# Kernel tuning notes

Measured on AMD Instinct MI355X. Metric: run time of the kernel, lower is better.

Reference implementation:

```python
import jax, jax.numpy as jnp
import numpy as np


def swish(x):
    return x * jax.nn.sigmoid(x)


def setup_inputs() -> dict:
    key = jax.random.key(0)
    ks = jax.random.split(key, 12)
    b, n, c, h, dg, hid = 4, 512, 256, 8, 6, 16

    def lin(k, i, o):
        return jax.random.normal(k, (i, o), jnp.float32) / np.float32(np.sqrt(i))

    return {
        "pairwise_g": jax.random.normal(ks[0], (b, n, n, dg), jnp.float32),
        "coset_functions": jax.random.normal(ks[1], (b, n, c), jnp.float32),
        "fc_q_w": lin(ks[2], c, c), "fc_q_b": jnp.zeros((c,), jnp.float32),
        "fc_k_w": lin(ks[3], c, c), "fc_k_b": jnp.zeros((c,), jnp.float32),
        "in_w": lin(ks[4], c, c), "in_b": jnp.zeros((c,), jnp.float32),
        "out_w": lin(ks[5], c, c), "out_b": jnp.zeros((c,), jnp.float32),
        "loc_w1": jax.random.normal(ks[6], (h, dg, hid), jnp.float32) / np.float32(np.sqrt(dg)),
        "loc_b1": jnp.zeros((h, hid), jnp.float32),
        "loc_w2": jax.random.normal(ks[7], (h, hid, hid), jnp.float32) / np.float32(np.sqrt(hid)),
        "loc_b2": jnp.zeros((h, hid), jnp.float32),
        "loc_w3": jax.random.normal(ks[8], (h, hid, 1), jnp.float32) / np.float32(np.sqrt(hid)),
        "loc_b3": jnp.zeros((h, 1), jnp.float32),
        "mask": jax.random.randint(ks[9], (4, 512), 0, 2) > 0,
    }


def reference(pairwise_g, coset_functions, fc_q_w, fc_q_b, fc_k_w, fc_k_b,
              in_w, in_b, out_w, out_b,
              loc_w1, loc_b1, loc_w2, loc_b2, loc_w3, loc_b3, mask):
    # nbhd_idx = arange(n) in the original (dense neighborhoods), so all
    # advanced-index gathers are identities and are expressed as broadcasts.
    b, n, c = coset_functions.shape
    h = loc_w1.shape[0]
    d = c // h

    # DotProductKernel: scores scaled by sqrt(embed_dim) = sqrt(c)
    Q = (coset_functions @ fc_q_w + fc_q_b).reshape(b, n, h, d)
    K = (coset_functions @ fc_k_w + fc_k_b).reshape(b, n, h, d)
    A_feat = jnp.einsum('bnhd,bmhd->bnmh', Q, K) / np.float32(np.sqrt(c))  # (b,n,m,h)

    # MultiheadWeightNet location kernel: per-head 3-layer MLP with swish
    # after every linear (LieConv-style LinearBNact blocks), out_dim=1.
    x = swish(jnp.einsum('bnmg,hgk->bnmhk', pairwise_g, loc_w1) + loc_b1)
    x = swish(jnp.einsum('bnmhk,hkj->bnmhj', x, loc_w2) + loc_b2)
    A_loc = swish(jnp.einsum('bnmhk,hko->bnmho', x, loc_w3) + loc_b3)[..., 0]  # (b,n,m,h)

    pre = A_loc + A_feat
    nbhd_mask = mask[:, None, :, None]          # mask over keys j: (b,1,m,1)
    pre = jnp.where(nbhd_mask, pre, jnp.float32(-1e38))
    att = jax.nn.softmax(pre, axis=2)           # softmax over neighbor dim m

    V = (coset_functions @ in_w + in_b).reshape(b, n, h, d)  # input_linear
    out = jnp.einsum('bnmh,bmhd->bnhd', att, V).reshape(b, n, c)
    return out @ out_w + out_b                  # output_linear; (b,n,c_out)
```

## Files before the change

### kernel.cpp

```cpp
#include <hip/hip_runtime.h>
#include <math.h>

namespace {

constexpr int kB = 4, kN = 512, kC = 256, kH = 8, kDG = 6, kHID = 16;

typedef _Float16 half2v __attribute__((ext_vector_type(2)));

__device__ __forceinline__ float swishf(float x) {
    return x * __builtin_amdgcn_rcpf(1.0f + __expf(-x));
}

__device__ __forceinline__ unsigned pk16(float a, float b) {
    unsigned short ha = __builtin_bit_cast(unsigned short, (_Float16)a);
    unsigned short hb = __builtin_bit_cast(unsigned short, (_Float16)b);
    return (unsigned)ha | ((unsigned)hb << 16);
}

__device__ __forceinline__ unsigned pkrtz(float a, float b) {
#if __has_builtin(__builtin_amdgcn_cvt_pkrtz)
    return __builtin_bit_cast(unsigned, __builtin_amdgcn_cvt_pkrtz(a, b));
#else
    return pk16(a, b);
#endif
}

__device__ __forceinline__ float fdot2u(unsigned a, unsigned b, float c) {
#if __has_builtin(__builtin_amdgcn_fdot2)
    return __builtin_amdgcn_fdot2(__builtin_bit_cast(half2v, a),
                                  __builtin_bit_cast(half2v, b), c, false);
#else
    half2v ha = __builtin_bit_cast(half2v, a);
    half2v hb = __builtin_bit_cast(half2v, b);
    return c + (float)ha[0] * (float)hb[0] + (float)ha[1] * (float)hb[1];
#endif
}

__global__ __launch_bounds__(256) void k_qkvc(
    const float* __restrict__ x,
    const float* __restrict__ wq, const float* __restrict__ bq,
    const float* __restrict__ wk, const float* __restrict__ bk,
    const float* __restrict__ wv, const float* __restrict__ bv,
    unsigned* __restrict__ Qh, unsigned* __restrict__ Kh,
    float* __restrict__ V,
    const unsigned char* __restrict__ mraw,
    int* __restrict__ list, int* __restrict__ meta) {
    const int t = threadIdx.x;

    if (blockIdx.x == 512) {
        __shared__ int s_isbool;
        if (t == 0) s_isbool = 0;
        __syncthreads();
        int found = 0;
        for (int i = t; i < kB * kN; i += 256)
            if ((i & 3) && mraw[i]) found = 1;
        if (found) atomicOr(&s_isbool, 1);
        __syncthreads();
        const int isb = s_isbool;
        const int b = t >> 6, lane = t & 63;
        const int* mi = (const int*)mraw;
        int base = 0;
        for (int c = 0; c < 8; ++c) {
            const int m = c * 64 + lane;
            const int idx = b * kN + m;
            const int valid = isb ? (mraw[idx] != 0) : (mi[idx] != 0);
            unsigned long long bal = __ballot(valid);
            int rank = (int)__popcll(bal & ((1ull << lane) - 1ull));
            if (valid) list[b * kN + base + rank] = m;
            base += (int)__popcll(bal);
        }
        for (int i = base + lane; i < kN; i += 64)
            list[b * kN + i] = (base == 0) ? i : 0;
        if (lane == 0) {
            meta[b] = (base == 0) ? kN : base;
            meta[4 + b] = (base == 0);
        }
        return;
    }

    __shared__ float sx[4][kC];
    const int r0 = blockIdx.x * 4;
    #pragma unroll
    for (int r = 0; r < 4; ++r) sx[r][t] = x[(r0 + r) * kC + t];
    __syncthreads();
    float aq[4] = {}, ak[4] = {}, av[4] = {};
    for (int k = 0; k < kC; ++k) {
        const float q = wq[k * kC + t];
        const float kk = wk[k * kC + t];
        const float v = wv[k * kC + t];
        #pragma unroll
        for (int r = 0; r < 4; ++r) {
            aq[r] += sx[r][k] * q;
            ak[r] += sx[r][k] * kk;
            av[r] += sx[r][k] * v;
        }
    }
    const float qb = bq[t], kb = bk[t], vb = bv[t];
    #pragma unroll
    for (int r = 0; r < 4; ++r) {
        const float qv = aq[r] + qb;
        const float kv = ak[r] + kb;
        V[(r0 + r) * kC + t] = av[r] + vb;
        const float qn = __shfl_down(qv, 1);
        const float kn = __shfl_down(kv, 1);
        if ((t & 1) == 0) {
            Qh[(r0 + r) * (kC / 2) + (t >> 1)] = pk16(qv, qn);
            Kh[(r0 + r) * (kC / 2) + (t >> 1)] = pk16(kv, kn);
        }
    }
}

__global__ __launch_bounds__(256, 6) void k_attn(
    const float* __restrict__ G,
    const unsigned* __restrict__ Qh,
    const unsigned* __restrict__ Kh,
    const float* __restrict__ V,
    const float* __restrict__ w1, const float* __restrict__ b1,
    const float* __restrict__ w2, const float* __restrict__ b2,
    const float* __restrict__ w3, const float* __restrict__ b3,
    const int* __restrict__ list, const int* __restrict__ meta,
    float* __restrict__ out) {
    __shared__ __align__(16) unsigned sQh[kC / 2];
    __shared__ __align__(16) unsigned sG[kN][4];
    __shared__ int sList[kN];
    __shared__ __align__(16) unsigned sW1[kH][kHID][4];
    __shared__ __align__(16) unsigned sW2[kH][kHID][8];
    __shared__ float sB1[kH][kHID];
    __shared__ float sB2[kH][kHID];
    __shared__ float sW3[kH][kHID];
    __shared__ float sB3[kH];
    __shared__ float sAtt[kH][kN];
    __shared__ float sInv[kH];

    const int bn = blockIdx.x;
    const int b = bn >> 9;
    const int t = threadIdx.x;

    if (t < kC / 2) sQh[t] = Qh[bn * (kC / 2) + t];
    sList[t] = list[b * kN + t];
    sList[t + 256] = list[b * kN + t + 256];
    #pragma unroll 1
    for (int rep = 0; rep < 2; ++rep) {
        const int m = t + rep * 256;
        const float* gp = G + ((size_t)bn * kN + m) * kDG;
        uint4 gw;
        gw.x = pkrtz(gp[0], gp[1]);
        gw.y = pkrtz(gp[2], gp[3]);
        gw.z = pkrtz(gp[4], gp[5]);
        gw.w = 0;
        *(uint4*)&sG[m][0] = gw;
    }
    if (t < 128) {
        const int h = t >> 4, k = t & 15;
        const float* wp = w1 + (h * kDG) * kHID + k;
        sW1[h][k][0] = pk16(wp[0], wp[16]);
        sW1[h][k][1] = pk16(wp[32], wp[48]);
        sW1[h][k][2] = pk16(wp[64], wp[80]);
        sW1[h][k][3] = 0;
        sB1[h][k] = b1[h * kHID + k];
        sB2[h][k] = b2[h * kHID + k];
        sW3[h][k] = w3[h * kHID + k];
    } else {
        const int t2 = t - 128;
        const int h = t2 >> 4, j = t2 & 15;
        const float* wp = w2 + h * kHID * kHID + j;
        #pragma unroll
        for (int kp = 0; kp < 8; ++kp)
            sW2[h][j][kp] = pk16(wp[(2 * kp) * kHID], wp[(2 * kp + 1) * kHID]);
        if (j == 0) sB3[h] = b3[h];
    }
    const int nv = meta[b];
    const int allm = meta[4 + b];
    __syncthreads();

    #pragma unroll 1
    for (int rep = 0; rep < 2; ++rep) {
        const int mc = t + rep * 256;
        if (mc < nv) {
            const int m = sList[mc];
            const uint4 gw = *(const uint4*)&sG[m][0];
            const unsigned* khrow = Kh + ((size_t)b * kN + m) * (kC / 2);
            #pragma unroll 1
            for (int h = 0; h < kH; ++h) {
                float af = 0.f;
                const uint4* kh4 = (const uint4*)(khrow + h * 16);
                const uint4* qh4 = (const uint4*)&sQh[h * 16];
                #pragma unroll
                for (int i = 0; i < 4; ++i) {
                    const uint4 kv = kh4[i];
                    const uint4 qv = qh4[i];
                    af = fdot2u(kv.x, qv.x, af);
                    af = fdot2u(kv.y, qv.y, af);
                    af = fdot2u(kv.z, qv.z, af);
                    af = fdot2u(kv.w, qv.w, af);
                }
                unsigned xp[8];
                #pragma unroll
                for (int k2 = 0; k2 < 8; ++k2) {
                    const uint4 wa = *(const uint4*)&sW1[h][2 * k2][0];
                    const uint4 wb = *(const uint4*)&sW1[h][2 * k2 + 1][0];
                    float aa = sB1[h][2 * k2], ab = sB1[h][2 * k2 + 1];
                    aa = fdot2u(gw.x, wa.x, aa);
                    aa = fdot2u(gw.y, wa.y, aa);
                    aa = fdot2u(gw.z, wa.z, aa);
                    ab = fdot2u(gw.x, wb.x, ab);
                    ab = fdot2u(gw.y, wb.y, ab);
                    ab = fdot2u(gw.z, wb.z, ab);
                    xp[k2] = pkrtz(swishf(aa), swishf(ab));
                }
                float a3 = sB3[h];
                #pragma unroll
                for (int j = 0; j < kHID; ++j) {
                    const uint4 w0 = ((const uint4*)&sW2[h][j][0])[0];
                    const uint4 w1q = ((const uint4*)&sW2[h][j][0])[1];
                    float acc = sB2[h][j];
                    acc = fdot2u(xp[0], w0.x, acc);
                    acc = fdot2u(xp[1], w0.y, acc);
                    acc = fdot2u(xp[2], w0.z, acc);
                    acc = fdot2u(xp[3], w0.w, acc);
                    acc = fdot2u(xp[4], w1q.x, acc);
                    acc = fdot2u(xp[5], w1q.y, acc);
                    acc = fdot2u(xp[6], w1q.z, acc);
                    acc = fdot2u(xp[7], w1q.w, acc);
                    a3 += swishf(acc) * sW3[h][j];
                }
                sAtt[h][mc] = allm ? 0.f : (swishf(a3) + af * 0.0625f);
            }
        }
    }
    __syncthreads();

    {
        const int hg = t >> 5;
        const int lane = t & 31;
        const int nv4 = (nv + 3) & ~3;
        float mx = -3.4e38f;
        for (int idx = lane; idx < nv; idx += 32)
            mx = fmaxf(mx, sAtt[hg][idx]);
        #pragma unroll
        for (int off = 16; off; off >>= 1)
            mx = fmaxf(mx, __shfl_xor(mx, off));
        float ls = 0.f;
        for (int idx = lane; idx < nv4; idx += 32) {
            const float e = (idx < nv) ? __expf(sAtt[hg][idx] - mx) : 0.f;
            sAtt[hg][idx] = e;
            ls += e;
        }
        #pragma unroll
        for (int off = 16; off; off >>= 1)
            ls += __shfl_xor(ls, off);
        if (lane == 0) sInv[hg] = 1.0f / ls;
    }
    __syncthreads();

    {
        const int h = t >> 5;
        const int dd = t & 31;
        const int nv4 = (nv + 3) & ~3;
        const float* vb = V + (size_t)b * kN * kC + h * 32 + dd;
        float a0 = 0.f, a1 = 0.f, a2 = 0.f, a3 = 0.f;
        for (int mc = 0; mc < nv4; mc += 4) {
            a0 += sAtt[h][mc + 0] * vb[(size_t)sList[mc + 0] * kC];
            a1 += sAtt[h][mc + 1] * vb[(size_t)sList[mc + 1] * kC];
            a2 += sAtt[h][mc + 2] * vb[(size_t)sList[mc + 2] * kC];
            a3 += sAtt[h][mc + 3] * vb[(size_t)sList[mc + 3] * kC];
        }
        out[bn * kC + t] = ((a0 + a1) + (a2 + a3)) * sInv[h];
    }
}

__global__ __launch_bounds__(256) void k_proj(
    const float* __restrict__ x,
    const float* __restrict__ w, const float* __restrict__ bias,
    float* __restrict__ y) {
    __shared__ float sx[8][kC];
    const int r0 = blockIdx.x * 8;
    const int t = threadIdx.x;
    #pragma unroll
    for (int r = 0; r < 8; ++r) sx[r][t] = x[(r0 + r) * kC + t];
    __syncthreads();
    float acc[8] = {};
    for (int k = 0; k < kC; ++k) {
        const float wv = w[k * kC + t];
        #pragma unroll
        for (int r = 0; r < 8; ++r) acc[r] += sx[r][k] * wv;
    }
    const float bb = bias[t];
    #pragma unroll
    for (int r = 0; r < 8; ++r) y[(r0 + r) * kC + t] = acc[r] + bb;
}

}

extern "C" void kernel_launch(void* const* d_in, const int* in_sizes, int n_in,
                              void* d_out, int out_size, void* d_ws, size_t ws_size,
                              hipStream_t stream) {
    (void)in_sizes; (void)n_in; (void)out_size; (void)ws_size;
    const float* G  = (const float*)d_in[0];
    const float* cf = (const float*)d_in[1];
    const float* wq = (const float*)d_in[2];
    const float* bq = (const float*)d_in[3];
    const float* wk = (const float*)d_in[4];
    const float* bk = (const float*)d_in[5];
    const float* wv = (const float*)d_in[6];
    const float* bv = (const float*)d_in[7];
    const float* wo = (const float*)d_in[8];
    const float* bo = (const float*)d_in[9];
    const float* w1 = (const float*)d_in[10];
    const float* b1 = (const float*)d_in[11];
    const float* w2 = (const float*)d_in[12];
    const float* b2 = (const float*)d_in[13];
    const float* w3 = (const float*)d_in[14];
    const float* b3 = (const float*)d_in[15];
    const unsigned char* mraw = (const unsigned char*)d_in[16];

    const int rows = kB * kN;
    unsigned* Qh = (unsigned*)d_ws;
    unsigned* Kh = Qh + (size_t)rows * (kC / 2);
    float* V = (float*)(Kh + (size_t)rows * (kC / 2));
    float* O = V + (size_t)rows * kC;
    int* list = (int*)(O + (size_t)rows * kC);
    int* meta = list + rows;

    k_qkvc<<<513, 256, 0, stream>>>(cf, wq, bq, wk, bk, wv, bv,
                                    Qh, Kh, V, mraw, list, meta);
    k_attn<<<rows, 256, 0, stream>>>(G, Qh, Kh, V, w1, b1, w2, b2, w3, b3,
                                     list, meta, O);
    k_proj<<<rows / 8, 256, 0, stream>>>(O, wo, bo, (float*)d_out);
}
```

Before: 264.3 us.

## Flatten key-head work items across threads and pad shared arrays against bank conflicts

The attention score loop now gives each thread one (key, head) pair from a flattened list of nv*8 items, where before each thread looped over all 8 heads for a key. This balances work when nv is not a multiple of 256 and lets the K loads and weight reads proceed without the serial head loop. Shared arrays (Q, W1, W2, biases, attention scores) get padded row strides so that threads in a wavefront touching different heads avoid LDS bank conflicts. The occupancy hint is lowered from 6 to 4 blocks, which lets the compiler use more registers but may reduce latency hiding. Adjacent lanes now read weights from different heads, so LDS broadcast of a shared address is lost.

```diff
diff --git a/kernel.cpp b/kernel.cpp
--- a/kernel.cpp
+++ b/kernel.cpp
@@ -4,6 +4,12 @@
 namespace {
 
 constexpr int kB = 4, kN = 512, kC = 256, kH = 8, kDG = 6, kHID = 16;
+
+constexpr int S_QH = 20;
+constexpr int S_W1 = 68;
+constexpr int S_W2 = 132;
+constexpr int S_B  = 17;
+constexpr int S_AT = 516;
 
 typedef _Float16 half2v __attribute__((ext_vector_type(2)));
 
@@ -110,7 +116,7 @@
     }
 }
 
-__global__ __launch_bounds__(256, 6) void k_attn(
+__global__ __launch_bounds__(256, 4) void k_attn(
     const float* __restrict__ G,
     const unsigned* __restrict__ Qh,
     const unsigned* __restrict__ Kh,
@@ -120,23 +126,26 @@
     const float* __restrict__ w3, const float* __restrict__ b3,
     const int* __restrict__ list, const int* __restrict__ meta,
     float* __restrict__ out) {
-    __shared__ __align__(16) unsigned sQh[kC / 2];
-    __shared__ __align__(16) unsigned sG[kN][4];
+    __shared__ __align__(16) unsigned sQh[kH * S_QH];
+    __shared__ __align__(16) uint4 sG4[kN];
     __shared__ int sList[kN];
-    __shared__ __align__(16) unsigned sW1[kH][kHID][4];
-    __shared__ __align__(16) unsigned sW2[kH][kHID][8];
-    __shared__ float sB1[kH][kHID];
-    __shared__ float sB2[kH][kHID];
-    __shared__ float sW3[kH][kHID];
+    __shared__ __align__(16) unsigned sW1[kH * S_W1];
+    __shared__ __align__(16) unsigned sW2[kH * S_W2];
+    __shared__ float sB1[kH * S_B];
+    __shared__ float sB2[kH * S_B];
+    __shared__ float sW3[kH * S_B];
     __shared__ float sB3[kH];
-    __shared__ float sAtt[kH][kN];
+    __shared__ float sAtt[kH * S_AT];
     __shared__ float sInv[kH];
 
     const int bn = blockIdx.x;
     const int b = bn >> 9;
     const int t = threadIdx.x;
 
-    if (t < kC / 2) sQh[t] = Qh[bn * (kC / 2) + t];
+    if (t < kH * S_QH) {
+        const int h = t / S_QH, r = t % S_QH;
+        sQh[t] = (r < 16) ? Qh[bn * (kC / 2) + h * 16 + r] : 0u;
+    }
     sList[t] = list[b * kN + t];
     sList[t + 256] = list[b * kN + t + 256];
     #pragma unroll 1
@@ -148,84 +157,82 @@
         gw.y = pkrtz(gp[2], gp[3]);
         gw.z = pkrtz(gp[4], gp[5]);
         gw.w = 0;
-        *(uint4*)&sG[m][0] = gw;
+        sG4[m] = gw;
     }
     if (t < 128) {
         const int h = t >> 4, k = t & 15;
         const float* wp = w1 + (h * kDG) * kHID + k;
-        sW1[h][k][0] = pk16(wp[0], wp[16]);
-        sW1[h][k][1] = pk16(wp[32], wp[48]);
-        sW1[h][k][2] = pk16(wp[64], wp[80]);
-        sW1[h][k][3] = 0;
-        sB1[h][k] = b1[h * kHID + k];
-        sB2[h][k] = b2[h * kHID + k];
-        sW3[h][k] = w3[h * kHID + k];
+        sW1[h * S_W1 + k * 4 + 0] = pk16(wp[0], wp[16]);
+        sW1[h * S_W1 + k * 4 + 1] = pk16(wp[32], wp[48]);
+        sW1[h * S_W1 + k * 4 + 2] = pk16(wp[64], wp[80]);
+        sW1[h * S_W1 + k * 4 + 3] = 0;
+        sB1[h * S_B + k] = b1[h * kHID + k];
+        sB2[h * S_B + k] = b2[h * kHID + k];
+        sW3[h * S_B + k] = w3[h * kHID + k];
     } else {
         const int t2 = t - 128;
         const int h = t2 >> 4, j = t2 & 15;
         const float* wp = w2 + h * kHID * kHID + j;
         #pragma unroll
         for (int kp = 0; kp < 8; ++kp)
-            sW2[h][j][kp] = pk16(wp[(2 * kp) * kHID], wp[(2 * kp + 1) * kHID]);
+            sW2[h * S_W2 + j * 8 + kp] = pk16(wp[(2 * kp) * kHID], wp[(2 * kp + 1) * kHID]);
         if (j == 0) sB3[h] = b3[h];
     }
     const int nv = meta[b];
     const int allm = meta[4 + b];
     __syncthreads();
 
+    const int items = nv * kH;
     #pragma unroll 1
-    for (int rep = 0; rep < 2; ++rep) {
-        const int mc = t + rep * 256;
-        if (mc < nv) {
+    for (int base = 0; base < items; base += 256) {
+        const int idx = base + t;
+        if (idx < items) {
+            const int h = idx & 7;
+            const int mc = idx >> 3;
             const int m = sList[mc];
-            const uint4 gw = *(const uint4*)&sG[m][0];
-            const unsigned* khrow = Kh + ((size_t)b * kN + m) * (kC / 2);
-            #pragma unroll 1
-            for (int h = 0; h < kH; ++h) {
-                float af = 0.f;
-                const uint4* kh4 = (const uint4*)(khrow + h * 16);
-                const uint4* qh4 = (const uint4*)&sQh[h * 16];
-                #pragma unroll
-                for (int i = 0; i < 4; ++i) {
-                    const uint4 kv = kh4[i];
-                    const uint4 qv = qh4[i];
-                    af = fdot2u(kv.x, qv.x, af);
-                    af = fdot2u(kv.y, qv.y, af);
-                    af = fdot2u(kv.z, qv.z, af);
-                    af = fdot2u(kv.w, qv.w, af);
-                }
-                unsigned xp[8];
-                #pragma unroll
-                for (int k2 = 0; k2 < 8; ++k2) {
-                    const uint4 wa = *(const uint4*)&sW1[h][2 * k2][0];
-                    const uint4 wb = *(const uint4*)&sW1[h][2 * k2 + 1][0];
-                    float aa = sB1[h][2 * k2], ab = sB1[h][2 * k2 + 1];
-                    aa = fdot2u(gw.x, wa.x, aa);
-                    aa = fdot2u(gw.y, wa.y, aa);
-                    aa = fdot2u(gw.z, wa.z, aa);
-                    ab = fdot2u(gw.x, wb.x, ab);
-                    ab = fdot2u(gw.y, wb.y, ab);
-                    ab = fdot2u(gw.z, wb.z, ab);
-                    xp[k2] = pkrtz(swishf(aa), swishf(ab));
-                }
-                float a3 = sB3[h];
-                #pragma unroll
-                for (int j = 0; j < kHID; ++j) {
-                    const uint4 w0 = ((const uint4*)&sW2[h][j][0])[0];
-                    const uint4 w1q = ((const uint4*)&sW2[h][j][0])[1];
-                    float acc = sB2[h][j];
-                    acc = fdot2u(xp[0], w0.x, acc);
-                    acc = fdot2u(xp[1], w0.y, acc);
-                    acc = fdot2u(xp[2], w0.z, acc);
-                    acc = fdot2u(xp[3], w0.w, acc);
-                    acc = fdot2u(xp[4], w1q.x, acc);
-                    acc = fdot2u(xp[5], w1q.y, acc);
-                    acc = fdot2u(xp[6], w1q.z, acc);
-                    acc = fdot2u(xp[7], w1q.w, acc);
-                    a3 += swishf(acc) * sW3[h][j];
-                }
-                sAtt[h][mc] = allm ? 0.f : (swishf(a3) + af * 0.0625f);
+            const uint4 gw = sG4[m];
+            const unsigned* khrow = Kh + ((size_t)(b * kN) + m) * (kC / 2) + h * 16;
+            float af = 0.f;
+            #pragma unroll
+            for (int i = 0; i < 4; ++i) {
+                const uint4 kv = ((const uint4*)khrow)[i];
+                const uint4 qv = *(const uint4*)&sQh[h * S_QH + 4 * i];
+                af = fdot2u(kv.x, qv.x, af);
+                af = fdot2u(kv.y, qv.y, af);
+                af = fdot2u(kv.z, qv.z, af);
+                af = fdot2u(kv.w, qv.w, af);
             }
+            unsigned xp[8];
+            #pragma unroll
+            for (int k2 = 0; k2 < 8; ++k2) {
+                const uint4 wa = *(const uint4*)&sW1[h * S_W1 + (2 * k2) * 4];
+                const uint4 wb = *(const uint4*)&sW1[h * S_W1 + (2 * k2 + 1) * 4];
+                float aa = sB1[h * S_B + 2 * k2], ab = sB1[h * S_B + 2 * k2 + 1];
+                aa = fdot2u(gw.x, wa.x, aa);
+                aa = fdot2u(gw.y, wa.y, aa);
+                aa = fdot2u(gw.z, wa.z, aa);
+                ab = fdot2u(gw.x, wb.x, ab);
+                ab = fdot2u(gw.y, wb.y, ab);
+                ab = fdot2u(gw.z, wb.z, ab);
+                xp[k2] = pkrtz(swishf(aa), swishf(ab));
+            }
+            float a3 = sB3[h];
+            #pragma unroll
+            for (int j = 0; j < kHID; ++j) {
+                const uint4 w0 = *(const uint4*)&sW2[h * S_W2 + j * 8];
+                const uint4 w1q = *(const uint4*)&sW2[h * S_W2 + j * 8 + 4];
+                float acc = sB2[h * S_B + j];
+                acc = fdot2u(xp[0], w0.x, acc);
+                acc = fdot2u(xp[1], w0.y, acc);
+                acc = fdot2u(xp[2], w0.z, acc);
+                acc = fdot2u(xp[3], w0.w, acc);
+                acc = fdot2u(xp[4], w1q.x, acc);
+                acc = fdot2u(xp[5], w1q.y, acc);
+                acc = fdot2u(xp[6], w1q.z, acc);
+                acc = fdot2u(xp[7], w1q.w, acc);
+                a3 += swishf(acc) * sW3[h * S_B + j];
+            }
+            sAtt[h * S_AT + mc] = allm ? 0.f : (swishf(a3) + af * 0.0625f);
         }
     }
     __syncthreads();
@@ -236,14 +243,14 @@
         const int nv4 = (nv + 3) & ~3;
         float mx = -3.4e38f;
         for (int idx = lane; idx < nv; idx += 32)
-            mx = fmaxf(mx, sAtt[hg][idx]);
+            mx = fmaxf(mx, sAtt[hg * S_AT + idx]);
         #pragma unroll
         for (int off = 16; off; off >>= 1)
             mx = fmaxf(mx, __shfl_xor(mx, off));
         float ls = 0.f;
         for (int idx = lane; idx < nv4; idx += 32) {
-            const float e = (idx < nv) ? __expf(sAtt[hg][idx] - mx) : 0.f;
-            sAtt[hg][idx] = e;
+            const float e = (idx < nv) ? __expf(sAtt[hg * S_AT + idx] - mx) : 0.f;
+            sAtt[hg * S_AT + idx] = e;
             ls += e;
         }
         #pragma unroll
@@ -260,10 +267,10 @@
         const float* vb = V + (size_t)b * kN * kC + h * 32 + dd;
         float a0 = 0.f, a1 = 0.f, a2 = 0.f, a3 = 0.f;
         for (int mc = 0; mc < nv4; mc += 4) {
-            a0 += sAtt[h][mc + 0] * vb[(size_t)sList[mc + 0] * kC];
-            a1 += sAtt[h][mc + 1] * vb[(size_t)sList[mc + 1] * kC];
-            a2 += sAtt[h][mc + 2] * vb[(size_t)sList[mc + 2] * kC];
-            a3 += sAtt[h][mc + 3] * vb[(size_t)sList[mc + 3] * kC];
+            a0 += sAtt[h * S_AT + mc + 0] * vb[(size_t)sList[mc + 0] * kC];
+            a1 += sAtt[h * S_AT + mc + 1] * vb[(size_t)sList[mc + 1] * kC];
+            a2 += sAtt[h * S_AT + mc + 2] * vb[(size_t)sList[mc + 2] * kC];
+            a3 += sAtt[h * S_AT + mc + 3] * vb[(size_t)sList[mc + 3] * kC];
         }
         out[bn * kC + t] = ((a0 + a1) + (a2 + a3)) * sInv[h];
     }
```

New measurement: 248.8 us. -5.9%, faster.
